# Performance work log

Hardware: AMD Instinct MI355X
Metric: run time of the kernel (lower is better)

The kernel has to match this reference:

```python
import jax, jax.numpy as jnp
import numpy as np

H = W = 64      # input_resolution
WS = 8          # window_size
SS = 4          # shift_size
DIM = 96
HEADS = 4
HEAD_DIM = DIM // HEADS
SCALE = HEAD_DIM ** -0.5
N = WS * WS     # tokens per window
EPS = 1e-5


def _rel_pos_index():
    # static (N, N) int index into the (2*WS-1)^2 bias table
    coords = np.stack(np.meshgrid(np.arange(WS), np.arange(WS), indexing='ij'))  # (2, WS, WS)
    cf = coords.reshape(2, -1)                       # (2, N)
    rel = (cf[:, :, None] - cf[:, None, :]).transpose(1, 2, 0)  # (N, N, 2)
    rel[:, :, 0] += WS - 1
    rel[:, :, 1] += WS - 1
    rel[:, :, 0] *= 2 * WS - 1
    return rel.sum(-1)                               # (N, N)


def _attn_mask():
    # static (nW, N, N) 0/-100 mask for shifted windows
    img = np.zeros((H, W))
    cnt = 0
    sl = (slice(0, -WS), slice(-WS, -SS), slice(-SS, None))
    for hs in sl:
        for ws_ in sl:
            img[hs, ws_] = cnt
            cnt += 1
    mw = img.reshape(H // WS, WS, W // WS, WS).transpose(0, 2, 1, 3).reshape(-1, N)
    diff = mw[:, None, :] - mw[:, :, None]
    return np.where(diff != 0, -100.0, 0.0).astype(np.float32)


_RPI = jnp.asarray(_rel_pos_index())
_MASK = jnp.asarray(_attn_mask())  # (nW, N, N)


def _layernorm(x, g, b):
    mu = jnp.mean(x, axis=-1, keepdims=True)
    var = jnp.mean(jnp.square(x - mu), axis=-1, keepdims=True)
    return (x - mu) * jax.lax.rsqrt(var + EPS) * g + b


def setup_inputs() -> dict:
    key = jax.random.key(0)
    ks = jax.random.split(key, 8)
    s = 0.02
    return {
        'x': jax.random.normal(ks[0], (64, H * W, DIM), jnp.float32),
        'norm1_g': jnp.ones((DIM,), jnp.float32),
        'norm1_b': jnp.zeros((DIM,), jnp.float32),
        'qkv_w': jax.random.normal(ks[1], (3 * DIM, DIM), jnp.float32) * s,
        'qkv_b': jnp.zeros((3 * DIM,), jnp.float32),
        'rel_bias_table': jax.random.normal(ks[2], ((2 * WS - 1) ** 2, HEADS), jnp.float32) * s,
        'proj_w': jax.random.normal(ks[3], (DIM, DIM), jnp.float32) * s,
        'proj_b': jnp.zeros((DIM,), jnp.float32),
        'norm2_g': jnp.ones((DIM,), jnp.float32),
        'norm2_b': jnp.zeros((DIM,), jnp.float32),
        'fc1_w': jax.random.normal(ks[4], (4 * DIM, DIM), jnp.float32) * s,
        'fc1_b': jnp.zeros((4 * DIM,), jnp.float32),
        'fc2_w': jax.random.normal(ks[5], (DIM, 4 * DIM), jnp.float32) * s,
        'fc2_b': jnp.zeros((DIM,), jnp.float32),
    }


def reference(x, norm1_g, norm1_b, qkv_w, qkv_b, rel_bias_table, proj_w, proj_b,
              norm2_g, norm2_b, fc1_w, fc1_b, fc2_w, fc2_b):
    B, L, C = x.shape
    nW = (H // WS) * (W // WS)
    shortcut = x

    h = _layernorm(x, norm1_g, norm1_b).reshape(B, H, W, C)
    h = jnp.roll(h, (-SS, -SS), axis=(1, 2))
    # window partition -> (B*nW, N, C)
    h = h.reshape(B, H // WS, WS, W // WS, WS, C).transpose(0, 1, 3, 2, 4, 5)
    h = h.reshape(B * nW, N, C)

    qkv = h @ qkv_w.T + qkv_b                                   # (B_, N, 3C)
    qkv = qkv.reshape(B * nW, N, 3, HEADS, HEAD_DIM).transpose(2, 0, 3, 1, 4)
    q, k, v = qkv[0] * SCALE, qkv[1], qkv[2]                    # (B_, heads, N, hd)

    attn = jnp.einsum('whnd,whmd->whnm', q, k)                  # (B_, heads, N, N)
    bias = rel_bias_table[_RPI.reshape(-1)].reshape(N, N, HEADS).transpose(2, 0, 1)
    attn = attn + bias[None]
    attn = attn.reshape(B, nW, HEADS, N, N) + _MASK[None, :, None]
    attn = jax.nn.softmax(attn.reshape(B * nW, HEADS, N, N), axis=-1)

    out = jnp.einsum('whnm,whmd->whnd', attn, v)                # (B_, heads, N, hd)
    out = out.transpose(0, 2, 1, 3).reshape(B * nW, N, C)
    out = out @ proj_w.T + proj_b

    # window reverse + un-shift
    out = out.reshape(B, H // WS, W // WS, WS, WS, C).transpose(0, 1, 3, 2, 4, 5)
    out = out.reshape(B, H, W, C)
    out = jnp.roll(out, (SS, SS), axis=(1, 2)).reshape(B, L, C)

    x = shortcut + out
    h2 = _layernorm(x, norm2_g, norm2_b)
    h2 = jax.nn.gelu(h2 @ fc1_w.T + fc1_b, approximate=False)
    h2 = h2 @ fc2_w.T + fc2_b
    return x + h2
```

## Files before the change

kernel.cpp:

```cpp
#include <hip/hip_runtime.h>
#include <hip/hip_fp16.h>
#include <math.h>

typedef _Float16 half_t;
typedef _Float16 half8 __attribute__((ext_vector_type(8)));
typedef float f32x4 __attribute__((ext_vector_type(4)));

#define MFMA(a, b, c) __builtin_amdgcn_mfma_f32_16x16x32_f16((a), (b), (c), 0, 0, 0)

static constexpr float kScale = 0.2041241452319315f;
static constexpr int RS   = 104;
static constexpr int QSTR = 200;
static constexpr int VTS  = 72;
static constexpr int PS   = 72;
static constexpr int H1S  = 392;

__global__ __launch_bounds__(256) void k_convert(const float* __restrict__ qkv_w,
                                                 const float* __restrict__ proj_w,
                                                 const float* __restrict__ fc1_w,
                                                 const float* __restrict__ fc2_w,
                                                 half_t* __restrict__ wbuf) {
  int i = blockIdx.x * 256 + threadIdx.x;
  if (i < 27648)       wbuf[i] = (half_t)qkv_w[i];
  else if (i < 36864)  wbuf[i] = (half_t)proj_w[i - 27648];
  else if (i < 73728)  wbuf[i] = (half_t)fc1_w[i - 36864];
  else                 wbuf[i] = (half_t)fc2_w[i - 73728];
}

__global__ __launch_bounds__(256, 3) void k_swin(
    const float* __restrict__ x,
    const float* __restrict__ n1g, const float* __restrict__ n1b,
    const half_t* __restrict__ qkvw, const float* __restrict__ qkv_b,
    const float* __restrict__ tbl_g, const half_t* __restrict__ projw,
    const float* __restrict__ proj_b,
    const float* __restrict__ n2g, const float* __restrict__ n2b,
    const half_t* __restrict__ fc1w, const float* __restrict__ fc1b,
    const half_t* __restrict__ fc2w, const float* __restrict__ fc2b,
    float* __restrict__ out) {
  __shared__ __attribute__((aligned(16))) unsigned char smem[52736];
  half_t* qbuf = (half_t*)smem;
  half_t* h1h  = (half_t*)smem;
  half_t* vT   = (half_t*)(smem + 25600);
  half_t* rbuf = (half_t*)(smem + 25600);
  half_t* hn   = (half_t*)(smem + 39424);
  half_t* pbuf = (half_t*)(smem + 39424);
  half_t* xn   = (half_t*)(smem + 39424);

  int tid = threadIdx.x;
  int wave = tid >> 6, lane = tid & 63;
  int l15 = lane & 15, quad = lane >> 4;
  int blk = blockIdx.x;
  int bb = blk >> 6, wh = (blk >> 3) & 7, ww = blk & 7;

  {
    int tok = wave * 16 + l15;
    float gg[24], bv[24];
#pragma unroll
    for (int kt = 0; kt < 3; ++kt) {
      int c0 = kt * 32 + quad * 8;
      float4 g0 = *(const float4*)(n1g + c0);
      float4 g1 = *(const float4*)(n1g + c0 + 4);
      float4 b0 = *(const float4*)(n1b + c0);
      float4 b1 = *(const float4*)(n1b + c0 + 4);
      gg[kt*8+0]=g0.x; gg[kt*8+1]=g0.y; gg[kt*8+2]=g0.z; gg[kt*8+3]=g0.w;
      gg[kt*8+4]=g1.x; gg[kt*8+5]=g1.y; gg[kt*8+6]=g1.z; gg[kt*8+7]=g1.w;
      bv[kt*8+0]=b0.x; bv[kt*8+1]=b0.y; bv[kt*8+2]=b0.z; bv[kt*8+3]=b0.w;
      bv[kt*8+4]=b1.x; bv[kt*8+5]=b1.y; bv[kt*8+6]=b1.z; bv[kt*8+7]=b1.w;
    }
    int sr = (wh * 8 + (tok >> 3) + 4) & 63;
    int sc = (ww * 8 + (tok & 7) + 4) & 63;
    const float* rp = x + ((size_t)bb * 4096 + sr * 64 + sc) * 96;
    float v[24];
    float s1 = 0.f, s2 = 0.f;
#pragma unroll
    for (int kt = 0; kt < 3; ++kt) {
      float4 a = *(const float4*)(rp + kt * 32 + quad * 8);
      float4 b = *(const float4*)(rp + kt * 32 + quad * 8 + 4);
      v[kt*8+0]=a.x; v[kt*8+1]=a.y; v[kt*8+2]=a.z; v[kt*8+3]=a.w;
      v[kt*8+4]=b.x; v[kt*8+5]=b.y; v[kt*8+6]=b.z; v[kt*8+7]=b.w;
    }
#pragma unroll
    for (int c = 0; c < 24; ++c) { s1 += v[c]; s2 += v[c] * v[c]; }
    s1 += __shfl_xor(s1, 16); s1 += __shfl_xor(s1, 32);
    s2 += __shfl_xor(s2, 16); s2 += __shfl_xor(s2, 32);
    float mu = s1 * (1.f / 96.f);
    float inv = rsqrtf(fmaxf(s2 * (1.f / 96.f) - mu * mu, 0.f) + 1e-5f);
#pragma unroll
    for (int kt = 0; kt < 3; ++kt) {
      half8 hh;
#pragma unroll
      for (int j = 0; j < 8; ++j)
        hh[j] = (half_t)((v[kt*8+j] - mu) * inv * gg[kt*8+j] + bv[kt*8+j]);
      *(half8*)(&hn[tok * RS + kt * 32 + quad * 8]) = hh;
    }
  }
  __syncthreads();

  {
    half8 af[4][3];
#pragma unroll
    for (int g = 0; g < 4; ++g)
#pragma unroll
      for (int kt = 0; kt < 3; ++kt)
        af[g][kt] = *(const half8*)(&hn[(g * 16 + l15) * RS + kt * 32 + quad * 8]);
    for (int t = wave; t < 18; t += 4) {
      half8 bf[3];
#pragma unroll
      for (int kt = 0; kt < 3; ++kt)
        bf[kt] = *(const half8*)(qkvw + (size_t)(t * 16 + l15) * 96 + kt * 32 + quad * 8);
      f32x4 acc[4] = {{0,0,0,0},{0,0,0,0},{0,0,0,0},{0,0,0,0}};
#pragma unroll
      for (int kt = 0; kt < 3; ++kt)
#pragma unroll
        for (int g = 0; g < 4; ++g)
          acc[g] = MFMA(af[g][kt], bf[kt], acc[g]);
      int col = t * 16 + l15;
      float bias = qkv_b[col];
      if (t < 12) {
        float sc_ = (t < 6) ? kScale : 1.f;
#pragma unroll
        for (int g = 0; g < 4; ++g)
#pragma unroll
          for (int r = 0; r < 4; ++r)
            qbuf[(g * 16 + quad * 4 + r) * QSTR + col] = (half_t)((acc[g][r] + bias) * sc_);
      } else {
        int vc = col - 192;
        int hd = vc / 24, c = vc - hd * 24;
#pragma unroll
        for (int g = 0; g < 4; ++g)
#pragma unroll
          for (int r = 0; r < 4; ++r)
            vT[hd * 24 * VTS + c * VTS + g * 16 + quad * 4 + r] = (half_t)(acc[g][r] + bias);
      }
    }
  }
  __syncthreads();

  f32x4 oacc[4][2];
  float inv_[4][4];
  {
    int head = wave;
    const half8 z8 = {};
    half8 qa[4], kb[4], vb[2][2];
#pragma unroll
    for (int g = 0; g < 4; ++g) {
      half8 t = *(const half8*)(&qbuf[(g * 16 + l15) * QSTR + head * 24 + quad * 8]);
      qa[g] = (quad < 3) ? t : z8;
    }
#pragma unroll
    for (int nt = 0; nt < 4; ++nt) {
      half8 t = *(const half8*)(&qbuf[(nt * 16 + l15) * QSTR + 96 + head * 24 + quad * 8]);
      kb[nt] = (quad < 3) ? t : z8;
    }
#pragma unroll
    for (int nt = 0; nt < 2; ++nt)
#pragma unroll
      for (int kt = 0; kt < 2; ++kt)
        vb[nt][kt] = *(const half8*)(&vT[head * 24 * VTS + (nt * 16 + l15) * VTS + kt * 32 + quad * 8]);

    float s[4][4][4];
#pragma unroll
    for (int g = 0; g < 4; ++g)
#pragma unroll
      for (int nt = 0; nt < 4; ++nt) {
        f32x4 a = {0, 0, 0, 0};
        a = MFMA(qa[g], kb[nt], a);
#pragma unroll
        for (int r = 0; r < 4; ++r) s[g][nt][r] = a[r];
      }

    int rj[4], jh_[4], jw_[4];
#pragma unroll
    for (int nt = 0; nt < 4; ++nt) {
      int j = nt * 16 + l15;
      jh_[nt] = j >> 3; jw_[nt] = j & 7;
      int rr = wh * 8 + jh_[nt], cc = ww * 8 + jw_[nt];
      rj[nt] = ((rr < 56) ? 0 : ((rr < 60) ? 1 : 2)) * 3 + ((cc < 56) ? 0 : ((cc < 60) ? 1 : 2));
    }
#pragma unroll
    for (int g = 0; g < 4; ++g)
#pragma unroll
      for (int r = 0; r < 4; ++r) {
        int i = g * 16 + quad * 4 + r;
        int ih = i >> 3, iw = i & 7;
        int rr = wh * 8 + ih, cc = ww * 8 + iw;
        int ri = ((rr < 56) ? 0 : ((rr < 60) ? 1 : 2)) * 3 + ((cc < 56) ? 0 : ((cc < 60) ? 1 : 2));
#pragma unroll
        for (int nt = 0; nt < 4; ++nt) {
          float val = s[g][nt][r] +
              tbl_g[((ih - jh_[nt] + 7) * 15 + (iw - jw_[nt] + 7)) * 4 + head];
          if (ri != rj[nt]) val -= 100.f;
          s[g][nt][r] = val;
        }
        float mx = fmaxf(fmaxf(s[g][0][r], s[g][1][r]), fmaxf(s[g][2][r], s[g][3][r]));
        mx = fmaxf(mx, __shfl_xor(mx, 1));
        mx = fmaxf(mx, __shfl_xor(mx, 2));
        mx = fmaxf(mx, __shfl_xor(mx, 4));
        mx = fmaxf(mx, __shfl_xor(mx, 8));
        float sum = 0.f;
#pragma unroll
        for (int nt = 0; nt < 4; ++nt) {
          float e = __expf(s[g][nt][r] - mx);
          s[g][nt][r] = e;
          sum += e;
        }
        sum += __shfl_xor(sum, 1);
        sum += __shfl_xor(sum, 2);
        sum += __shfl_xor(sum, 4);
        sum += __shfl_xor(sum, 8);
        inv_[g][r] = 1.f / sum;
      }

    half_t* pb = pbuf + head * 16 * PS;
#pragma unroll
    for (int q4 = 0; q4 < 4; ++q4) {
#pragma unroll
      for (int nt = 0; nt < 4; ++nt)
#pragma unroll
        for (int r = 0; r < 4; ++r)
          pb[(quad * 4 + r) * PS + nt * 16 + l15] = (half_t)s[q4][nt][r];
      half8 pa[2];
#pragma unroll
      for (int kt = 0; kt < 2; ++kt)
        pa[kt] = *(const half8*)(&pb[l15 * PS + kt * 32 + quad * 8]);
#pragma unroll
      for (int nt = 0; nt < 2; ++nt) {
        f32x4 a = {0, 0, 0, 0};
#pragma unroll
        for (int kt = 0; kt < 2; ++kt) a = MFMA(pa[kt], vb[nt][kt], a);
        oacc[q4][nt] = a;
      }
    }
  }
  __syncthreads();
  {
    int head = wave;
#pragma unroll
    for (int q4 = 0; q4 < 4; ++q4)
#pragma unroll
      for (int nt = 0; nt < 2; ++nt)
#pragma unroll
        for (int r = 0; r < 4; ++r) {
          int c = nt * 16 + l15;
          if (c < 24)
            qbuf[(q4 * 16 + quad * 4 + r) * QSTR + head * 24 + c] =
                (half_t)(oacc[q4][nt][r] * inv_[q4][r]);
        }
  }
  __syncthreads();

  {
    half8 pa2[4][3];
#pragma unroll
    for (int g = 0; g < 4; ++g)
#pragma unroll
      for (int kt = 0; kt < 3; ++kt)
        pa2[g][kt] = *(const half8*)(&qbuf[(g * 16 + l15) * QSTR + kt * 32 + quad * 8]);
    for (int t = wave; t < 6; t += 4) {
      half8 bf[3];
#pragma unroll
      for (int kt = 0; kt < 3; ++kt)
        bf[kt] = *(const half8*)(projw + (size_t)(t * 16 + l15) * 96 + kt * 32 + quad * 8);
      f32x4 acc[4] = {{0,0,0,0},{0,0,0,0},{0,0,0,0},{0,0,0,0}};
#pragma unroll
      for (int kt = 0; kt < 3; ++kt)
#pragma unroll
        for (int g = 0; g < 4; ++g)
          acc[g] = MFMA(pa2[g][kt], bf[kt], acc[g]);
      int col = t * 16 + l15;
      float bias = proj_b[col];
#pragma unroll
      for (int g = 0; g < 4; ++g)
#pragma unroll
        for (int r = 0; r < 4; ++r) {
          int tok = g * 16 + quad * 4 + r;
          int sr = (wh * 8 + (tok >> 3) + 4) & 63;
          int sc = (ww * 8 + (tok & 7) + 4) & 63;
          size_t fidx = ((size_t)bb * 4096 + sr * 64 + sc) * 96 + col;
          rbuf[tok * RS + col] = (half_t)(x[fidx] + acc[g][r] + bias);
        }
    }
  }
  __syncthreads();

  {
    int r4 = wave * 16 + (lane >> 2);
    int ch = lane & 3;
    const half_t* rp = rbuf + r4 * RS + ch * 24;
    half8 w0 = *(const half8*)(rp);
    half8 w1 = *(const half8*)(rp + 8);
    half8 w2 = *(const half8*)(rp + 16);
    float v[24];
#pragma unroll
    for (int j = 0; j < 8; ++j) {
      v[j] = (float)w0[j]; v[j + 8] = (float)w1[j]; v[j + 16] = (float)w2[j];
    }
    float s1 = 0.f, s2 = 0.f;
#pragma unroll
    for (int j = 0; j < 24; ++j) { s1 += v[j]; s2 += v[j] * v[j]; }
    s1 += __shfl_xor(s1, 1); s1 += __shfl_xor(s1, 2);
    s2 += __shfl_xor(s2, 1); s2 += __shfl_xor(s2, 2);
    float mu = s1 * (1.f / 96.f);
    float inv = rsqrtf(fmaxf(s2 * (1.f / 96.f) - mu * mu, 0.f) + 1e-5f);
    float gv[24], bb2[24];
#pragma unroll
    for (int q = 0; q < 6; ++q) {
      float4 g4 = *(const float4*)(n2g + ch * 24 + q * 4);
      float4 b4 = *(const float4*)(n2b + ch * 24 + q * 4);
      gv[q*4+0]=g4.x; gv[q*4+1]=g4.y; gv[q*4+2]=g4.z; gv[q*4+3]=g4.w;
      bb2[q*4+0]=b4.x; bb2[q*4+1]=b4.y; bb2[q*4+2]=b4.z; bb2[q*4+3]=b4.w;
    }
    half_t* op = xn + r4 * RS + ch * 24;
#pragma unroll
    for (int q = 0; q < 3; ++q) {
      half8 h;
#pragma unroll
      for (int j = 0; j < 8; ++j)
        h[j] = (half_t)((v[q*8+j] - mu) * inv * gv[q*8+j] + bb2[q*8+j]);
      *(half8*)(op + q * 8) = h;
    }
  }
  __syncthreads();

  for (int hb = 0; hb < 2; ++hb) {
    {
      half8 a5[2][3];
#pragma unroll
      for (int g2 = 0; g2 < 2; ++g2)
#pragma unroll
        for (int kt = 0; kt < 3; ++kt)
          a5[g2][kt] = *(const half8*)(&xn[((hb * 2 + g2) * 16 + l15) * RS + kt * 32 + quad * 8]);
      for (int t = wave; t < 24; t += 4) {
        int n0 = t * 16 + l15;
        half8 bf[3];
#pragma unroll
        for (int kt = 0; kt < 3; ++kt)
          bf[kt] = *(const half8*)(fc1w + (size_t)n0 * 96 + kt * 32 + quad * 8);
        f32x4 acc[2] = {{0,0,0,0},{0,0,0,0}};
#pragma unroll
        for (int kt = 0; kt < 3; ++kt)
#pragma unroll
          for (int g2 = 0; g2 < 2; ++g2)
            acc[g2] = MFMA(a5[g2][kt], bf[kt], acc[g2]);
        float bias = fc1b[n0];
#pragma unroll
        for (int g2 = 0; g2 < 2; ++g2)
#pragma unroll
          for (int r = 0; r < 4; ++r) {
            float vv = acc[g2][r] + bias;
            vv = 0.5f * vv * (1.f + erff(vv * 0.70710678118f));
            h1h[(g2 * 16 + quad * 4 + r) * H1S + n0] = (half_t)vv;
          }
      }
    }
    __syncthreads();
    {
      int rt = wave >> 1, chh = wave & 1;
      half8 a2[12];
#pragma unroll
      for (int kt = 0; kt < 12; ++kt)
        a2[kt] = *(const half8*)(&h1h[(rt * 16 + l15) * H1S + kt * 32 + quad * 8]);
#pragma unroll
      for (int i = 0; i < 3; ++i) {
        int t = chh * 3 + i;
        f32x4 acc = {0, 0, 0, 0};
#pragma unroll
        for (int kt = 0; kt < 12; ++kt) {
          half8 bf = *(const half8*)(fc2w + (size_t)(t * 16 + l15) * 384 + kt * 32 + quad * 8);
          acc = MFMA(a2[kt], bf, acc);
        }
        int col = t * 16 + l15;
        float bias = fc2b[col];
#pragma unroll
        for (int r = 0; r < 4; ++r) {
          int tok = hb * 32 + rt * 16 + quad * 4 + r;
          int sr = (wh * 8 + (tok >> 3) + 4) & 63;
          int sc = (ww * 8 + (tok & 7) + 4) & 63;
          size_t fidx = ((size_t)bb * 4096 + sr * 64 + sc) * 96 + col;
          out[fidx] = (float)rbuf[tok * RS + col] + acc[r] + bias;
        }
      }
    }
    __syncthreads();
  }
}

extern "C" void kernel_launch(void* const* d_in, const int* in_sizes, int n_in,
                              void* d_out, int out_size, void* d_ws, size_t ws_size,
                              hipStream_t stream) {
  const float* x      = (const float*)d_in[0];
  const float* n1g    = (const float*)d_in[1];
  const float* n1b    = (const float*)d_in[2];
  const float* qkv_w  = (const float*)d_in[3];
  const float* qkv_b  = (const float*)d_in[4];
  const float* rtbl   = (const float*)d_in[5];
  const float* proj_w = (const float*)d_in[6];
  const float* proj_b = (const float*)d_in[7];
  const float* n2g    = (const float*)d_in[8];
  const float* n2b    = (const float*)d_in[9];
  const float* fc1_w  = (const float*)d_in[10];
  const float* fc1_b  = (const float*)d_in[11];
  const float* fc2_w  = (const float*)d_in[12];
  const float* fc2_b  = (const float*)d_in[13];
  float* out = (float*)d_out;

  if (ws_size < 221184) return;
  half_t* wbuf = (half_t*)d_ws;

  k_convert<<<432, 256, 0, stream>>>(qkv_w, proj_w, fc1_w, fc2_w, wbuf);
  k_swin<<<4096, 256, 0, stream>>>(x, n1g, n1b, wbuf, qkv_b, rtbl,
                                   wbuf + 27648, proj_b, n2g, n2b,
                                   wbuf + 36864, fc1_b, wbuf + 73728, fc2_b, out);
}
```

Before: 437.8 us.

## Restructure Swin block around per-wave token ownership with fewer block barriers

```diff
diff --git a/kernel.cpp b/kernel.cpp
--- a/kernel.cpp
+++ b/kernel.cpp
@@ -9,42 +9,44 @@
 #define MFMA(a, b, c) __builtin_amdgcn_mfma_f32_16x16x32_f16((a), (b), (c), 0, 0, 0)
 
 static constexpr float kScale = 0.2041241452319315f;
-static constexpr int RS   = 104;
 static constexpr int QSTR = 200;
 static constexpr int VTS  = 72;
-static constexpr int PS   = 72;
-static constexpr int H1S  = 392;
+static constexpr int XNS  = 104;
 
 __global__ __launch_bounds__(256) void k_convert(const float* __restrict__ qkv_w,
                                                  const float* __restrict__ proj_w,
                                                  const float* __restrict__ fc1_w,
                                                  const float* __restrict__ fc2_w,
-                                                 half_t* __restrict__ wbuf) {
+                                                 const float* __restrict__ tbl,
+                                                 half_t* __restrict__ wbuf,
+                                                 float* __restrict__ biasT) {
   int i = blockIdx.x * 256 + threadIdx.x;
-  if (i < 27648)       wbuf[i] = (half_t)qkv_w[i];
-  else if (i < 36864)  wbuf[i] = (half_t)proj_w[i - 27648];
-  else if (i < 73728)  wbuf[i] = (half_t)fc1_w[i - 36864];
-  else                 wbuf[i] = (half_t)fc2_w[i - 73728];
+  if (i < 27648)        wbuf[i] = (half_t)qkv_w[i];
+  else if (i < 36864)   wbuf[i] = (half_t)proj_w[i - 27648];
+  else if (i < 73728)   wbuf[i] = (half_t)fc1_w[i - 36864];
+  else if (i < 110592)  wbuf[i] = (half_t)fc2_w[i - 73728];
+  else if (biasT != nullptr) {
+    int j = i - 110592;
+    int h = j >> 12, rem = j & 4095;
+    int ii = rem >> 6, jj = rem & 63;
+    int ih = ii >> 3, iw = ii & 7, jh = jj >> 3, jw = jj & 7;
+    biasT[j] = tbl[((ih - jh + 7) * 15 + (iw - jw + 7)) * 4 + h];
+  }
 }
 
-__global__ __launch_bounds__(256, 3) void k_swin(
+__global__ __launch_bounds__(256, 4) void k_swin(
     const float* __restrict__ x,
     const float* __restrict__ n1g, const float* __restrict__ n1b,
     const half_t* __restrict__ qkvw, const float* __restrict__ qkv_b,
-    const float* __restrict__ tbl_g, const half_t* __restrict__ projw,
-    const float* __restrict__ proj_b,
+    const float* __restrict__ tbl_g, const float* __restrict__ biasT,
+    const half_t* __restrict__ projw, const float* __restrict__ proj_b,
     const float* __restrict__ n2g, const float* __restrict__ n2b,
     const half_t* __restrict__ fc1w, const float* __restrict__ fc1b,
     const half_t* __restrict__ fc2w, const float* __restrict__ fc2b,
     float* __restrict__ out) {
-  __shared__ __attribute__((aligned(16))) unsigned char smem[52736];
+  __shared__ __attribute__((aligned(16))) unsigned char smem[40640];
   half_t* qbuf = (half_t*)smem;
-  half_t* h1h  = (half_t*)smem;
-  half_t* vT   = (half_t*)(smem + 25600);
-  half_t* rbuf = (half_t*)(smem + 25600);
-  half_t* hn   = (half_t*)(smem + 39424);
-  half_t* pbuf = (half_t*)(smem + 39424);
-  half_t* xn   = (half_t*)(smem + 39424);
+  half_t* vbuf = (half_t*)(smem + 25600);
 
   int tid = threadIdx.x;
   int wave = tid >> 6, lane = tid & 63;
@@ -52,9 +54,27 @@
   int blk = blockIdx.x;
   int bb = blk >> 6, wh = (blk >> 3) & 7, ww = blk & 7;
 
+  half8 af[3];
   {
     int tok = wave * 16 + l15;
-    float gg[24], bv[24];
+    int sr = (wh * 8 + (tok >> 3) + 4) & 63;
+    int sc = (ww * 8 + (tok & 7) + 4) & 63;
+    const float* rp = x + ((size_t)bb * 4096 + sr * 64 + sc) * 96;
+    float v[24];
+    float s1 = 0.f, s2 = 0.f;
+#pragma unroll
+    for (int kt = 0; kt < 3; ++kt) {
+      float4 a = *(const float4*)(rp + kt * 32 + quad * 8);
+      float4 b = *(const float4*)(rp + kt * 32 + quad * 8 + 4);
+      v[kt*8+0]=a.x; v[kt*8+1]=a.y; v[kt*8+2]=a.z; v[kt*8+3]=a.w;
+      v[kt*8+4]=b.x; v[kt*8+5]=b.y; v[kt*8+6]=b.z; v[kt*8+7]=b.w;
+    }
+#pragma unroll
+    for (int c = 0; c < 24; ++c) { s1 += v[c]; s2 += v[c] * v[c]; }
+    s1 += __shfl_xor(s1, 16); s1 += __shfl_xor(s1, 32);
+    s2 += __shfl_xor(s2, 16); s2 += __shfl_xor(s2, 32);
+    float mu = s1 * (1.f / 96.f);
+    float inv = rsqrtf(fmaxf(s2 * (1.f / 96.f) - mu * mu, 0.f) + 1e-5f);
 #pragma unroll
     for (int kt = 0; kt < 3; ++kt) {
       int c0 = kt * 32 + quad * 8;
@@ -62,91 +82,49 @@
       float4 g1 = *(const float4*)(n1g + c0 + 4);
       float4 b0 = *(const float4*)(n1b + c0);
       float4 b1 = *(const float4*)(n1b + c0 + 4);
-      gg[kt*8+0]=g0.x; gg[kt*8+1]=g0.y; gg[kt*8+2]=g0.z; gg[kt*8+3]=g0.w;
-      gg[kt*8+4]=g1.x; gg[kt*8+5]=g1.y; gg[kt*8+6]=g1.z; gg[kt*8+7]=g1.w;
-      bv[kt*8+0]=b0.x; bv[kt*8+1]=b0.y; bv[kt*8+2]=b0.z; bv[kt*8+3]=b0.w;
-      bv[kt*8+4]=b1.x; bv[kt*8+5]=b1.y; bv[kt*8+6]=b1.z; bv[kt*8+7]=b1.w;
-    }
-    int sr = (wh * 8 + (tok >> 3) + 4) & 63;
-    int sc = (ww * 8 + (tok & 7) + 4) & 63;
-    const float* rp = x + ((size_t)bb * 4096 + sr * 64 + sc) * 96;
-    float v[24];
-    float s1 = 0.f, s2 = 0.f;
-#pragma unroll
-    for (int kt = 0; kt < 3; ++kt) {
-      float4 a = *(const float4*)(rp + kt * 32 + quad * 8);
-      float4 b = *(const float4*)(rp + kt * 32 + quad * 8 + 4);
-      v[kt*8+0]=a.x; v[kt*8+1]=a.y; v[kt*8+2]=a.z; v[kt*8+3]=a.w;
-      v[kt*8+4]=b.x; v[kt*8+5]=b.y; v[kt*8+6]=b.z; v[kt*8+7]=b.w;
-    }
-#pragma unroll
-    for (int c = 0; c < 24; ++c) { s1 += v[c]; s2 += v[c] * v[c]; }
-    s1 += __shfl_xor(s1, 16); s1 += __shfl_xor(s1, 32);
-    s2 += __shfl_xor(s2, 16); s2 += __shfl_xor(s2, 32);
-    float mu = s1 * (1.f / 96.f);
-    float inv = rsqrtf(fmaxf(s2 * (1.f / 96.f) - mu * mu, 0.f) + 1e-5f);
-#pragma unroll
-    for (int kt = 0; kt < 3; ++kt) {
+      float gg[8] = {g0.x,g0.y,g0.z,g0.w,g1.x,g1.y,g1.z,g1.w};
+      float bv[8] = {b0.x,b0.y,b0.z,b0.w,b1.x,b1.y,b1.z,b1.w};
       half8 hh;
 #pragma unroll
       for (int j = 0; j < 8; ++j)
-        hh[j] = (half_t)((v[kt*8+j] - mu) * inv * gg[kt*8+j] + bv[kt*8+j]);
-      *(half8*)(&hn[tok * RS + kt * 32 + quad * 8]) = hh;
-    }
-  }
-  __syncthreads();
+        hh[j] = (half_t)((v[kt*8+j] - mu) * inv * gg[j] + bv[j]);
+      af[kt] = hh;
+    }
+  }
 
   {
-    half8 af[4][3];
-#pragma unroll
-    for (int g = 0; g < 4; ++g)
-#pragma unroll
-      for (int kt = 0; kt < 3; ++kt)
-        af[g][kt] = *(const half8*)(&hn[(g * 16 + l15) * RS + kt * 32 + quad * 8]);
-    for (int t = wave; t < 18; t += 4) {
-      half8 bf[3];
-#pragma unroll
-      for (int kt = 0; kt < 3; ++kt)
-        bf[kt] = *(const half8*)(qkvw + (size_t)(t * 16 + l15) * 96 + kt * 32 + quad * 8);
-      f32x4 acc[4] = {{0,0,0,0},{0,0,0,0},{0,0,0,0},{0,0,0,0}};
-#pragma unroll
-      for (int kt = 0; kt < 3; ++kt)
-#pragma unroll
-        for (int g = 0; g < 4; ++g)
-          acc[g] = MFMA(af[g][kt], bf[kt], acc[g]);
-      int col = t * 16 + l15;
-      float bias = qkv_b[col];
+#pragma unroll
+    for (int t = 0; t < 18; ++t) {
+      int n0 = t * 16 + l15;
+      const half_t* wp = qkvw + (size_t)n0 * 96 + quad * 8;
+      half8 b0 = *(const half8*)(wp);
+      half8 b1 = *(const half8*)(wp + 32);
+      half8 b2 = *(const half8*)(wp + 64);
+      f32x4 acc = {0, 0, 0, 0};
+      acc = MFMA(af[0], b0, acc);
+      acc = MFMA(af[1], b1, acc);
+      acc = MFMA(af[2], b2, acc);
+      float bias = qkv_b[n0];
       if (t < 12) {
         float sc_ = (t < 6) ? kScale : 1.f;
 #pragma unroll
-        for (int g = 0; g < 4; ++g)
-#pragma unroll
-          for (int r = 0; r < 4; ++r)
-            qbuf[(g * 16 + quad * 4 + r) * QSTR + col] = (half_t)((acc[g][r] + bias) * sc_);
+        for (int r = 0; r < 4; ++r)
+          qbuf[(wave * 16 + quad * 4 + r) * QSTR + n0] = (half_t)((acc[r] + bias) * sc_);
       } else {
-        int vc = col - 192;
+        int vc = n0 - 192;
         int hd = vc / 24, c = vc - hd * 24;
 #pragma unroll
-        for (int g = 0; g < 4; ++g)
-#pragma unroll
-          for (int r = 0; r < 4; ++r)
-            vT[hd * 24 * VTS + c * VTS + g * 16 + quad * 4 + r] = (half_t)(acc[g][r] + bias);
+        for (int r = 0; r < 4; ++r)
+          vbuf[hd * 24 * VTS + c * VTS + wave * 16 + quad * 4 + r] = (half_t)(acc[r] + bias);
       }
     }
   }
   __syncthreads();
 
-  f32x4 oacc[4][2];
-  float inv_[4][4];
   {
     int head = wave;
     const half8 z8 = {};
-    half8 qa[4], kb[4], vb[2][2];
-#pragma unroll
-    for (int g = 0; g < 4; ++g) {
-      half8 t = *(const half8*)(&qbuf[(g * 16 + l15) * QSTR + head * 24 + quad * 8]);
-      qa[g] = (quad < 3) ? t : z8;
-    }
+    half8 kb[4], vb[2][2];
 #pragma unroll
     for (int nt = 0; nt < 4; ++nt) {
       half8 t = *(const half8*)(&qbuf[(nt * 16 + l15) * QSTR + 96 + head * 24 + quad * 8]);
@@ -156,18 +134,7 @@
     for (int nt = 0; nt < 2; ++nt)
 #pragma unroll
       for (int kt = 0; kt < 2; ++kt)
-        vb[nt][kt] = *(const half8*)(&vT[head * 24 * VTS + (nt * 16 + l15) * VTS + kt * 32 + quad * 8]);
-
-    float s[4][4][4];
-#pragma unroll
-    for (int g = 0; g < 4; ++g)
-#pragma unroll
-      for (int nt = 0; nt < 4; ++nt) {
-        f32x4 a = {0, 0, 0, 0};
-        a = MFMA(qa[g], kb[nt], a);
-#pragma unroll
-        for (int r = 0; r < 4; ++r) s[g][nt][r] = a[r];
-      }
+        vb[nt][kt] = *(const half8*)(&vbuf[head * 24 * VTS + (nt * 16 + l15) * VTS + kt * 32 + quad * 8]);
 
     int rj[4], jh_[4], jw_[4];
 #pragma unroll
@@ -177,22 +144,44 @@
       int rr = wh * 8 + jh_[nt], cc = ww * 8 + jw_[nt];
       rj[nt] = ((rr < 56) ? 0 : ((rr < 60) ? 1 : 2)) * 3 + ((cc < 56) ? 0 : ((cc < 60) ? 1 : 2));
     }
-#pragma unroll
-    for (int g = 0; g < 4; ++g)
+
+    half_t* pb = vbuf + head * 24 * VTS;
+    f32x4 oacc[4][2];
+
+#pragma unroll
+    for (int g2 = 0; g2 < 4; ++g2) {
+      half8 qt = *(const half8*)(&qbuf[(g2 * 16 + l15) * QSTR + head * 24 + quad * 8]);
+      half8 qa = (quad < 3) ? qt : z8;
+      f32x4 sv[4];
+#pragma unroll
+      for (int nt = 0; nt < 4; ++nt) {
+        f32x4 a = {0, 0, 0, 0};
+        sv[nt] = MFMA(qa, kb[nt], a);
+      }
+      float pinv[4];
 #pragma unroll
       for (int r = 0; r < 4; ++r) {
-        int i = g * 16 + quad * 4 + r;
+        int i = g2 * 16 + quad * 4 + r;
         int ih = i >> 3, iw = i & 7;
         int rr = wh * 8 + ih, cc = ww * 8 + iw;
         int ri = ((rr < 56) ? 0 : ((rr < 60) ? 1 : 2)) * 3 + ((cc < 56) ? 0 : ((cc < 60) ? 1 : 2));
+        float bvv[4];
+        if (biasT != nullptr) {
+          const float* bp = biasT + (head << 12) + (i << 6) + l15;
+#pragma unroll
+          for (int nt = 0; nt < 4; ++nt) bvv[nt] = bp[nt * 16];
+        } else {
+#pragma unroll
+          for (int nt = 0; nt < 4; ++nt)
+            bvv[nt] = tbl_g[((ih - jh_[nt] + 7) * 15 + (iw - jw_[nt] + 7)) * 4 + head];
+        }
 #pragma unroll
         for (int nt = 0; nt < 4; ++nt) {
-          float val = s[g][nt][r] +
-              tbl_g[((ih - jh_[nt] + 7) * 15 + (iw - jw_[nt] + 7)) * 4 + head];
+          float val = sv[nt][r] + bvv[nt];
           if (ri != rj[nt]) val -= 100.f;
-          s[g][nt][r] = val;
+          sv[nt][r] = val;
         }
-        float mx = fmaxf(fmaxf(s[g][0][r], s[g][1][r]), fmaxf(s[g][2][r], s[g][3][r]));
+        float mx = fmaxf(fmaxf(sv[0][r], sv[1][r]), fmaxf(sv[2][r], sv[3][r]));
         mx = fmaxf(mx, __shfl_xor(mx, 1));
         mx = fmaxf(mx, __shfl_xor(mx, 2));
         mx = fmaxf(mx, __shfl_xor(mx, 4));
@@ -200,188 +189,159 @@
         float sum = 0.f;
 #pragma unroll
         for (int nt = 0; nt < 4; ++nt) {
-          float e = __expf(s[g][nt][r] - mx);
-          s[g][nt][r] = e;
+          float e = __expf(sv[nt][r] - mx);
+          sv[nt][r] = e;
           sum += e;
         }
         sum += __shfl_xor(sum, 1);
         sum += __shfl_xor(sum, 2);
         sum += __shfl_xor(sum, 4);
         sum += __shfl_xor(sum, 8);
-        inv_[g][r] = 1.f / sum;
-      }
-
-    half_t* pb = pbuf + head * 16 * PS;
-#pragma unroll
-    for (int q4 = 0; q4 < 4; ++q4) {
+        pinv[r] = __builtin_amdgcn_rcpf(sum);
+      }
 #pragma unroll
       for (int nt = 0; nt < 4; ++nt)
 #pragma unroll
         for (int r = 0; r < 4; ++r)
-          pb[(quad * 4 + r) * PS + nt * 16 + l15] = (half_t)s[q4][nt][r];
-      half8 pa[2];
-#pragma unroll
-      for (int kt = 0; kt < 2; ++kt)
-        pa[kt] = *(const half8*)(&pb[l15 * PS + kt * 32 + quad * 8]);
+          pb[(quad * 4 + r) * VTS + nt * 16 + l15] = (half_t)(sv[nt][r] * pinv[r]);
+      __builtin_amdgcn_sched_barrier(0);
+      half8 pa0 = *(const half8*)(&pb[l15 * VTS + quad * 8]);
+      half8 pa1 = *(const half8*)(&pb[l15 * VTS + 32 + quad * 8]);
 #pragma unroll
       for (int nt = 0; nt < 2; ++nt) {
         f32x4 a = {0, 0, 0, 0};
-#pragma unroll
-        for (int kt = 0; kt < 2; ++kt) a = MFMA(pa[kt], vb[nt][kt], a);
-        oacc[q4][nt] = a;
-      }
-    }
+        a = MFMA(pa0, vb[nt][0], a);
+        a = MFMA(pa1, vb[nt][1], a);
+        oacc[g2][nt] = a;
+      }
+    }
+#pragma unroll
+    for (int g2 = 0; g2 < 4; ++g2)
+#pragma unroll
+      for (int nt = 0; nt < 2; ++nt) {
+        int c = nt * 16 + l15;
+        if (c < 24)
+#pragma unroll
+          for (int r = 0; r < 4; ++r)
+            qbuf[(g2 * 16 + quad * 4 + r) * QSTR + head * 24 + c] = (half_t)oacc[g2][nt][r];
+      }
   }
   __syncthreads();
+
+  float rv[6][4];
+  int foff[4];
+  half8 a5[3];
   {
-    int head = wave;
-#pragma unroll
-    for (int q4 = 0; q4 < 4; ++q4)
-#pragma unroll
-      for (int nt = 0; nt < 2; ++nt)
-#pragma unroll
-        for (int r = 0; r < 4; ++r) {
-          int c = nt * 16 + l15;
-          if (c < 24)
-            qbuf[(q4 * 16 + quad * 4 + r) * QSTR + head * 24 + c] =
-                (half_t)(oacc[q4][nt][r] * inv_[q4][r]);
-        }
-  }
-  __syncthreads();
-
-  {
-    half8 pa2[4][3];
-#pragma unroll
-    for (int g = 0; g < 4; ++g)
-#pragma unroll
-      for (int kt = 0; kt < 3; ++kt)
-        pa2[g][kt] = *(const half8*)(&qbuf[(g * 16 + l15) * QSTR + kt * 32 + quad * 8]);
-    for (int t = wave; t < 6; t += 4) {
-      half8 bf[3];
-#pragma unroll
-      for (int kt = 0; kt < 3; ++kt)
-        bf[kt] = *(const half8*)(projw + (size_t)(t * 16 + l15) * 96 + kt * 32 + quad * 8);
-      f32x4 acc[4] = {{0,0,0,0},{0,0,0,0},{0,0,0,0},{0,0,0,0}};
-#pragma unroll
-      for (int kt = 0; kt < 3; ++kt)
-#pragma unroll
-        for (int g = 0; g < 4; ++g)
-          acc[g] = MFMA(pa2[g][kt], bf[kt], acc[g]);
-      int col = t * 16 + l15;
-      float bias = proj_b[col];
-#pragma unroll
-      for (int g = 0; g < 4; ++g)
-#pragma unroll
-        for (int r = 0; r < 4; ++r) {
-          int tok = g * 16 + quad * 4 + r;
-          int sr = (wh * 8 + (tok >> 3) + 4) & 63;
-          int sc = (ww * 8 + (tok & 7) + 4) & 63;
-          size_t fidx = ((size_t)bb * 4096 + sr * 64 + sc) * 96 + col;
-          rbuf[tok * RS + col] = (half_t)(x[fidx] + acc[g][r] + bias);
-        }
-    }
-  }
-  __syncthreads();
-
-  {
-    int r4 = wave * 16 + (lane >> 2);
-    int ch = lane & 3;
-    const half_t* rp = rbuf + r4 * RS + ch * 24;
-    half8 w0 = *(const half8*)(rp);
-    half8 w1 = *(const half8*)(rp + 8);
-    half8 w2 = *(const half8*)(rp + 16);
-    float v[24];
-#pragma unroll
-    for (int j = 0; j < 8; ++j) {
-      v[j] = (float)w0[j]; v[j + 8] = (float)w1[j]; v[j + 16] = (float)w2[j];
-    }
-    float s1 = 0.f, s2 = 0.f;
-#pragma unroll
-    for (int j = 0; j < 24; ++j) { s1 += v[j]; s2 += v[j] * v[j]; }
-    s1 += __shfl_xor(s1, 1); s1 += __shfl_xor(s1, 2);
-    s2 += __shfl_xor(s2, 1); s2 += __shfl_xor(s2, 2);
-    float mu = s1 * (1.f / 96.f);
-    float inv = rsqrtf(fmaxf(s2 * (1.f / 96.f) - mu * mu, 0.f) + 1e-5f);
-    float gv[24], bb2[24];
-#pragma unroll
-    for (int q = 0; q < 6; ++q) {
-      float4 g4 = *(const float4*)(n2g + ch * 24 + q * 4);
-      float4 b4 = *(const float4*)(n2b + ch * 24 + q * 4);
-      gv[q*4+0]=g4.x; gv[q*4+1]=g4.y; gv[q*4+2]=g4.z; gv[q*4+3]=g4.w;
-      bb2[q*4+0]=b4.x; bb2[q*4+1]=b4.y; bb2[q*4+2]=b4.z; bb2[q*4+3]=b4.w;
-    }
-    half_t* op = xn + r4 * RS + ch * 24;
-#pragma unroll
-    for (int q = 0; q < 3; ++q) {
-      half8 h;
-#pragma unroll
-      for (int j = 0; j < 8; ++j)
-        h[j] = (half_t)((v[q*8+j] - mu) * inv * gv[q*8+j] + bb2[q*8+j]);
-      *(half8*)(op + q * 8) = h;
-    }
-  }
-  __syncthreads();
-
-  for (int hb = 0; hb < 2; ++hb) {
-    {
-      half8 a5[2][3];
-#pragma unroll
-      for (int g2 = 0; g2 < 2; ++g2)
-#pragma unroll
-        for (int kt = 0; kt < 3; ++kt)
-          a5[g2][kt] = *(const half8*)(&xn[((hb * 2 + g2) * 16 + l15) * RS + kt * 32 + quad * 8]);
-      for (int t = wave; t < 24; t += 4) {
-        int n0 = t * 16 + l15;
-        half8 bf[3];
-#pragma unroll
-        for (int kt = 0; kt < 3; ++kt)
-          bf[kt] = *(const half8*)(fc1w + (size_t)n0 * 96 + kt * 32 + quad * 8);
-        f32x4 acc[2] = {{0,0,0,0},{0,0,0,0}};
-#pragma unroll
-        for (int kt = 0; kt < 3; ++kt)
-#pragma unroll
-          for (int g2 = 0; g2 < 2; ++g2)
-            acc[g2] = MFMA(a5[g2][kt], bf[kt], acc[g2]);
-        float bias = fc1b[n0];
-#pragma unroll
-        for (int g2 = 0; g2 < 2; ++g2)
-#pragma unroll
-          for (int r = 0; r < 4; ++r) {
-            float vv = acc[g2][r] + bias;
-            vv = 0.5f * vv * (1.f + erff(vv * 0.70710678118f));
-            h1h[(g2 * 16 + quad * 4 + r) * H1S + n0] = (half_t)vv;
-          }
-      }
-    }
-    __syncthreads();
-    {
-      int rt = wave >> 1, chh = wave & 1;
-      half8 a2[12];
-#pragma unroll
-      for (int kt = 0; kt < 12; ++kt)
-        a2[kt] = *(const half8*)(&h1h[(rt * 16 + l15) * H1S + kt * 32 + quad * 8]);
-#pragma unroll
-      for (int i = 0; i < 3; ++i) {
-        int t = chh * 3 + i;
-        f32x4 acc = {0, 0, 0, 0};
-#pragma unroll
-        for (int kt = 0; kt < 12; ++kt) {
-          half8 bf = *(const half8*)(fc2w + (size_t)(t * 16 + l15) * 384 + kt * 32 + quad * 8);
-          acc = MFMA(a2[kt], bf, acc);
-        }
-        int col = t * 16 + l15;
-        float bias = fc2b[col];
-#pragma unroll
-        for (int r = 0; r < 4; ++r) {
-          int tok = hb * 32 + rt * 16 + quad * 4 + r;
-          int sr = (wh * 8 + (tok >> 3) + 4) & 63;
-          int sc = (ww * 8 + (tok & 7) + 4) & 63;
-          size_t fidx = ((size_t)bb * 4096 + sr * 64 + sc) * 96 + col;
-          out[fidx] = (float)rbuf[tok * RS + col] + acc[r] + bias;
-        }
-      }
-    }
-    __syncthreads();
+    half8 oa[3];
+#pragma unroll
+    for (int kt = 0; kt < 3; ++kt)
+      oa[kt] = *(const half8*)(&qbuf[(wave * 16 + l15) * QSTR + kt * 32 + quad * 8]);
+    f32x4 acc[6];
+#pragma unroll
+    for (int t = 0; t < 6; ++t) {
+      int n0 = t * 16 + l15;
+      const half_t* wp = projw + (size_t)n0 * 96 + quad * 8;
+      half8 b0 = *(const half8*)(wp);
+      half8 b1 = *(const half8*)(wp + 32);
+      half8 b2 = *(const half8*)(wp + 64);
+      f32x4 a = {0, 0, 0, 0};
+      a = MFMA(oa[0], b0, a);
+      a = MFMA(oa[1], b1, a);
+      a = MFMA(oa[2], b2, a);
+      acc[t] = a;
+    }
+    float xv[6][4];
+#pragma unroll
+    for (int r = 0; r < 4; ++r) {
+      int tok = wave * 16 + quad * 4 + r;
+      int sr = (wh * 8 + (tok >> 3) + 4) & 63;
+      int sc = (ww * 8 + (tok & 7) + 4) & 63;
+      foff[r] = (bb * 4096 + sr * 64 + sc) * 96 + l15;
+      const float* xp = x + foff[r];
+#pragma unroll
+      for (int t = 0; t < 6; ++t) xv[t][r] = xp[t * 16];
+    }
+    float s1[4] = {0, 0, 0, 0}, s2[4] = {0, 0, 0, 0};
+#pragma unroll
+    for (int t = 0; t < 6; ++t) {
+      float pbv = proj_b[t * 16 + l15];
+#pragma unroll
+      for (int r = 0; r < 4; ++r) {
+        float vvv = xv[t][r] + acc[t][r] + pbv;
+        rv[t][r] = vvv;
+        s1[r] += vvv; s2[r] += vvv * vvv;
+      }
+    }
+    float mu[4], nv[4];
+#pragma unroll
+    for (int r = 0; r < 4; ++r) {
+      s1[r] += __shfl_xor(s1[r], 1); s1[r] += __shfl_xor(s1[r], 2);
+      s1[r] += __shfl_xor(s1[r], 4); s1[r] += __shfl_xor(s1[r], 8);
+      s2[r] += __shfl_xor(s2[r], 1); s2[r] += __shfl_xor(s2[r], 2);
+      s2[r] += __shfl_xor(s2[r], 4); s2[r] += __shfl_xor(s2[r], 8);
+      mu[r] = s1[r] * (1.f / 96.f);
+      nv[r] = rsqrtf(fmaxf(s2[r] * (1.f / 96.f) - mu[r] * mu[r], 0.f) + 1e-5f);
+    }
+    half_t* xnb = vbuf;
+#pragma unroll
+    for (int t = 0; t < 6; ++t) {
+      int n0 = t * 16 + l15;
+      float gv = n2g[n0], bv = n2b[n0];
+#pragma unroll
+      for (int r = 0; r < 4; ++r)
+        xnb[(wave * 16 + quad * 4 + r) * XNS + n0] =
+            (half_t)((rv[t][r] - mu[r]) * nv[r] * gv + bv);
+    }
+    __builtin_amdgcn_sched_barrier(0);
+#pragma unroll
+    for (int kt = 0; kt < 3; ++kt)
+      a5[kt] = *(const half8*)(&xnb[(wave * 16 + l15) * XNS + kt * 32 + quad * 8]);
+  }
+
+  f32x4 acc6[6];
+#pragma unroll
+  for (int t = 0; t < 6; ++t) acc6[t] = (f32x4){0, 0, 0, 0};
+#pragma unroll 1
+  for (int kb = 0; kb < 2; ++kb) {
+#pragma unroll
+    for (int th = 0; th < 12; ++th) {
+      int n0 = (kb * 12 + th) * 16 + l15;
+      const half_t* wp = fc1w + (size_t)n0 * 96 + quad * 8;
+      half8 b0 = *(const half8*)(wp);
+      half8 b1 = *(const half8*)(wp + 32);
+      half8 b2 = *(const half8*)(wp + 64);
+      f32x4 a = {0, 0, 0, 0};
+      a = MFMA(a5[0], b0, a);
+      a = MFMA(a5[1], b1, a);
+      a = MFMA(a5[2], b2, a);
+      float fb = fc1b[n0];
+#pragma unroll
+      for (int r = 0; r < 4; ++r) {
+        float vvv = a[r] + fb;
+        float u = vvv * (1.5957691216f + 0.1427096322f * vvv * vvv);
+        float g = vvv * __builtin_amdgcn_rcpf(1.f + __expf(-u));
+        qbuf[(wave * 16 + quad * 4 + r) * QSTR + th * 16 + l15] = (half_t)g;
+      }
+    }
+    __builtin_amdgcn_sched_barrier(0);
+#pragma unroll
+    for (int kk = 0; kk < 6; ++kk) {
+      half8 ha = *(const half8*)(&qbuf[(wave * 16 + l15) * QSTR + kk * 32 + quad * 8]);
+#pragma unroll
+      for (int t6 = 0; t6 < 6; ++t6) {
+        half8 bf = *(const half8*)(fc2w + (size_t)(t6 * 16 + l15) * 384 + kb * 192 + kk * 32 + quad * 8);
+        acc6[t6] = MFMA(ha, bf, acc6[t6]);
+      }
+    }
+    __builtin_amdgcn_sched_barrier(0);
+  }
+
+#pragma unroll
+  for (int t6 = 0; t6 < 6; ++t6) {
+    float fb = fc2b[t6 * 16 + l15];
+#pragma unroll
+    for (int r = 0; r < 4; ++r)
+      out[(size_t)foff[r] + t6 * 16] = rv[t6][r] + acc6[t6][r] + fb;
   }
 }
 
@@ -406,9 +366,10 @@
 
   if (ws_size < 221184) return;
   half_t* wbuf = (half_t*)d_ws;
-
-  k_convert<<<432, 256, 0, stream>>>(qkv_w, proj_w, fc1_w, fc2_w, wbuf);
-  k_swin<<<4096, 256, 0, stream>>>(x, n1g, n1b, wbuf, qkv_b, rtbl,
+  float* biasT = (ws_size >= 221184 + 65536) ? (float*)((char*)d_ws + 221184) : nullptr;
+
+  k_convert<<<496, 256, 0, stream>>>(qkv_w, proj_w, fc1_w, fc2_w, rtbl, wbuf, biasT);
+  k_swin<<<4096, 256, 0, stream>>>(x, n1g, n1b, wbuf, qkv_b, rtbl, biasT,
                                    wbuf + 27648, proj_b, n2g, n2b,
                                    wbuf + 36864, fc1_b, wbuf + 73728, fc2_b, out);
 }
```

After: 468.5 us. 7.0% more time.
